# Kernel tuning notes

Hardware: AMD Instinct MI355X
Metric: run time of the kernel (lower is better)

## Reference

```python
import jax, jax.numpy as jnp
import numpy as np

B, E, C, N, NNZ = 64, 100000, 80000, 10000, 1600000
EPS = 1e-5  # GroupLayerNorm eps


def setup_inputs() -> dict:
    key = jax.random.key(0)
    ks = jax.random.split(key, 8)
    x = jax.random.normal(ks[0], (B, E), dtype=jnp.float32)
    # sparse layer nonzero coordinates (graph-structure-constrained weights)
    w_in_rows = jax.random.randint(ks[1], (NNZ,), 0, E)    # edge index (input dim)
    w_in_cols = jax.random.randint(ks[2], (NNZ,), 0, C)    # hidden channel index
    w_out_rows = jax.random.randint(ks[3], (NNZ,), 0, C)   # hidden channel index
    w_out_cols = jax.random.randint(ks[4], (NNZ,), 0, E)   # edge index (output dim)
    # xavier-like scale: avg fan_in per hidden channel ~ NNZ/C
    scale_in = np.sqrt(2.0 / (NNZ / C + NNZ / E)).astype(np.float32)
    v_in = jax.random.normal(ks[5], (NNZ,), dtype=jnp.float32) * scale_in
    v_out = jax.random.normal(ks[6], (NNZ,), dtype=jnp.float32) * scale_in
    b_in = jnp.zeros((C,), jnp.float32)
    b_out = jnp.zeros((E,), jnp.float32)
    gamma = jnp.ones((C,), jnp.float32)   # GroupLayerNorm affine scale (per channel)
    beta = jnp.zeros((C,), jnp.float32)   # GroupLayerNorm affine shift
    channel_groups = jnp.arange(C, dtype=jnp.int64) // (C // N)  # 8 channels per node
    return {
        'x': x, 'v_in': v_in, 'b_in': b_in, 'v_out': v_out, 'b_out': b_out,
        'gamma': gamma, 'beta': beta,
        'w_in_rows': w_in_rows, 'w_in_cols': w_in_cols,
        'w_out_rows': w_out_rows, 'w_out_cols': w_out_cols,
        'channel_groups': channel_groups,
    }


def _sparse_linear(x, rows, cols, values, bias, out_dim):
    # out[b, c] = sum_{k: cols[k]==c} x[b, rows[k]] * values[k] + bias[c]
    contrib = x[:, rows] * values  # [B, nnz]
    out = jnp.zeros((x.shape[0], out_dim), x.dtype).at[:, cols].add(contrib)
    return out + bias


def _group_layer_norm(h, groups, gamma, beta):
    # per-node-group layernorm over that node's channels
    Bsz = h.shape[0]
    counts = jnp.zeros((N,), h.dtype).at[groups].add(1.0)
    gsum = jnp.zeros((Bsz, N), h.dtype).at[:, groups].add(h)
    gsq = jnp.zeros((Bsz, N), h.dtype).at[:, groups].add(h * h)
    mean = gsum / counts
    var = gsq / counts - mean * mean
    hn = (h - mean[:, groups]) * jax.lax.rsqrt(var[:, groups] + EPS)
    return gamma * hn + beta


def reference(x, v_in, b_in, v_out, b_out, gamma, beta,
              w_in_rows, w_in_cols, w_out_rows, w_out_cols, channel_groups):
    # 1. input sparse linear: edges -> hidden channels
    h = _sparse_linear(x, w_in_rows, w_in_cols, v_in, b_in, C)
    # 2. norm_first=True: GroupLayerNorm then nonlinearity (ELU)
    h = _group_layer_norm(h, channel_groups, gamma, beta)
    h = jax.nn.elu(h)
    # 3. output sparse linear: hidden channels -> edges
    out = _sparse_linear(h, w_out_rows, w_out_cols, v_out, b_out, E)
    # 4. dropout p=0 (identity), residual
    return out + x
```

## Files before the change

### kernel.cpp

```cpp
#include <hip/hip_runtime.h>
#include <hip/hip_bf16.h>

#define B_   64
#define E_   100000
#define C_   80000
#define N_   10000
#define GS   8
#define NNZ_ 1600000
#define EPS_ 1e-5f

#define SHIFT 7
#define BK    128
#define NBLK  256
#define CHUNK (NNZ_ / NBLK)
#define NBMAX 800
#define SCAN_CHUNK 1024
#define SORTT 512

__global__ void transpose_x_kernel(const float* __restrict__ x, __hip_bfloat16* __restrict__ xT) {
    __shared__ float tile[64][65];
    const int e0 = blockIdx.x * 64;
    const int t  = threadIdx.x;
    const int c  = t & 63;
    const int r4 = t >> 6;
#pragma unroll
    for (int j = 0; j < 16; ++j) {
        int br = r4 * 16 + j;
        int e  = e0 + c;
        if (e < E_) tile[c][br] = x[br * E_ + e];
    }
    __syncthreads();
#pragma unroll
    for (int j = 0; j < 16; ++j) {
        int er = r4 * 16 + j;
        int e  = e0 + er;
        if (e < E_) xT[e * 64 + c] = __float2bfloat16(tile[er][c]);
    }
}

__global__ __launch_bounds__(SORTT) void count_kernel(const int* __restrict__ cols,
                                                      int* __restrict__ blkcnt, int nb) {
    __shared__ int hist[NBMAX];
    const int t = threadIdx.x;
    for (int j = t; j < nb; j += SORTT) hist[j] = 0;
    __syncthreads();
    const int base = blockIdx.x * CHUNK;
    const int end  = min(NNZ_, base + CHUNK);
    for (int k = base + t; k < end; k += SORTT)
        atomicAdd(&hist[cols[k] >> SHIFT], 1);
    __syncthreads();
    for (int j = t; j < nb; j += SORTT) blkcnt[j * NBLK + blockIdx.x] = hist[j];
}

__global__ void scan_partial_kernel(const int* __restrict__ counts, int* __restrict__ partials,
                                    int dim) {
    __shared__ int red[256];
    const int t    = threadIdx.x;
    const int base = blockIdx.x * SCAN_CHUNK + t * 4;
    int s = 0;
#pragma unroll
    for (int j = 0; j < 4; ++j) { int i = base + j; if (i < dim) s += counts[i]; }
    red[t] = s;
    __syncthreads();
    for (int d = 128; d > 0; d >>= 1) {
        if (t < d) red[t] += red[t + d];
        __syncthreads();
    }
    if (t == 0) partials[blockIdx.x] = red[0];
}

__global__ void scan_base_kernel(int* __restrict__ partials, int nparts) {
    __shared__ int buf[256];
    const int t = threadIdx.x;
    buf[t] = (t < nparts) ? partials[t] : 0;
    __syncthreads();
    for (int d = 1; d < 256; d <<= 1) {
        int v = (t >= d) ? buf[t - d] : 0;
        __syncthreads();
        buf[t] += v;
        __syncthreads();
    }
    if (t < nparts) partials[t] = (t == 0) ? 0 : buf[t - 1];
}

__global__ void scan_emit_kernel(const int* __restrict__ counts, const int* __restrict__ partials,
                                 int* __restrict__ bases, int dim) {
    __shared__ int red[256];
    const int t    = threadIdx.x;
    const int base = blockIdx.x * SCAN_CHUNK + t * 4;
    int v[4];
    int s = 0;
#pragma unroll
    for (int j = 0; j < 4; ++j) {
        int i = base + j;
        v[j] = (i < dim) ? counts[i] : 0;
        s += v[j];
    }
    red[t] = s;
    __syncthreads();
    for (int d = 1; d < 256; d <<= 1) {
        int u = (t >= d) ? red[t - d] : 0;
        __syncthreads();
        red[t] += u;
        __syncthreads();
    }
    int run = partials[blockIdx.x] + ((t == 0) ? 0 : red[t - 1]);
#pragma unroll
    for (int j = 0; j < 4; ++j) {
        int i = base + j;
        if (i < dim) bases[i] = run;
        run += v[j];
    }
}

__global__ __launch_bounds__(SORTT) void place_kernel(const int* __restrict__ rows,
                             const int* __restrict__ cols,
                             const float* __restrict__ vals, const int* __restrict__ bases,
                             uint2* __restrict__ binned, int nb) {
    __shared__ uint2 staged[CHUNK];
    __shared__ unsigned short bof[CHUNK];
    __shared__ int hist[NBMAX];
    __shared__ int cur[NBMAX];
    __shared__ int goff[NBMAX];
    __shared__ int red[SORTT];
    const int t    = threadIdx.x;
    const int blk  = blockIdx.x;
    const int base = blk * CHUNK;
    const int n    = min(NNZ_, base + CHUNK) - base;
    for (int j = t; j < nb; j += SORTT) hist[j] = 0;
    __syncthreads();
    for (int k = t; k < n; k += SORTT) atomicAdd(&hist[cols[base + k] >> SHIFT], 1);
    __syncthreads();
    int lv[2];
    int s = 0;
    const int b0 = t * 2;
#pragma unroll
    for (int j = 0; j < 2; ++j) {
        int idx = b0 + j;
        lv[j] = (idx < nb) ? hist[idx] : 0;
        s += lv[j];
    }
    red[t] = s;
    __syncthreads();
    for (int d = 1; d < SORTT; d <<= 1) {
        int v = (t >= d) ? red[t - d] : 0;
        __syncthreads();
        red[t] += v;
        __syncthreads();
    }
    int run = (t == 0) ? 0 : red[t - 1];
#pragma unroll
    for (int j = 0; j < 2; ++j) {
        int idx = b0 + j;
        if (idx < nb) {
            cur[idx]  = run;
            goff[idx] = bases[idx * NBLK + blk] - run;
        }
        run += lv[j];
    }
    __syncthreads();
    for (int k = t; k < n; k += SORTT) {
        const int c = cols[base + k];
        const int j = c >> SHIFT;
        const int p = atomicAdd(&cur[j], 1);
        staged[p] = make_uint2((unsigned)rows[base + k] | ((unsigned)(c & (BK - 1)) << 17),
                               __float_as_uint(vals[base + k]));
        bof[p] = (unsigned short)j;
    }
    __syncthreads();
    for (int k = t; k < n; k += SORTT) {
        const int j = bof[k];
        binned[goff[j] + k] = staged[k];
    }
}

__global__ __launch_bounds__(SORTT) void binsort_kernel(const uint2* __restrict__ binned,
                               const int* __restrict__ bases,
                               int* __restrict__ offsets, float2* __restrict__ csr,
                               int nb, int dim) {
    __shared__ int hist[BK];
    __shared__ int sc[BK];
    __shared__ int cur[BK];
    const int t   = threadIdx.x;
    const int bkt = blockIdx.x;
    if (t < BK) hist[t] = 0;
    __syncthreads();
    const int beg = bases[bkt * NBLK];
    const int end = (bkt + 1 < nb) ? bases[(bkt + 1) * NBLK] : NNZ_;
    for (int i = beg + t; i < end; i += SORTT)
        atomicAdd(&hist[binned[i].x >> 17], 1);
    __syncthreads();
    if (t < BK) sc[t] = hist[t];
    __syncthreads();
    for (int d = 1; d < BK; d <<= 1) {
        int v = (t < BK && t >= d) ? sc[t - d] : 0;
        __syncthreads();
        if (t < BK) sc[t] += v;
        __syncthreads();
    }
    if (t < BK) {
        const int ex = beg + ((t == 0) ? 0 : sc[t - 1]);
        cur[t] = ex;
        const int c = bkt * BK + t;
        if (c < dim) offsets[c] = ex;
    }
    if (t == 0 && bkt == nb - 1) offsets[dim] = NNZ_;
    __syncthreads();
    for (int i = beg + t; i < end; i += SORTT) {
        const uint2 e = binned[i];
        const int pos = atomicAdd(&cur[e.x >> 17], 1);
        csr[pos] = make_float2(__int_as_float((int)(e.x & 0x1FFFFu)), __uint_as_float(e.y));
    }
}

__device__ __forceinline__ float col_dot(const float2* __restrict__ csr,
                                         const __hip_bfloat16* __restrict__ src,
                                         int beg, int end, int lane, float a0i) {
    float a[16];
    a[0] = a0i;
#pragma unroll
    for (int j = 1; j < 16; ++j) a[j] = 0.f;
    for (int i0 = beg; i0 < end; i0 += 64) {
        const int m = min(64, end - i0);
        float2 mine = make_float2(0.f, 0.f);
        if (lane < m) mine = csr[i0 + lane];
        const int   mr = __float_as_int(mine.x);
        const int   mv = __float_as_int(mine.y);
        int e = 0;
        for (; e + 16 <= m; e += 16) {
#define GSTEP(J)                                                                        \
            {                                                                           \
                const int   r = __builtin_amdgcn_readlane(mr, e + (J));                 \
                const float v = __int_as_float(__builtin_amdgcn_readlane(mv, e + (J))); \
                a[J] = fmaf(v, __bfloat162float(src[r * 64 + lane]), a[J]);             \
            }
            GSTEP(0)  GSTEP(1)  GSTEP(2)  GSTEP(3)
            GSTEP(4)  GSTEP(5)  GSTEP(6)  GSTEP(7)
            GSTEP(8)  GSTEP(9)  GSTEP(10) GSTEP(11)
            GSTEP(12) GSTEP(13) GSTEP(14) GSTEP(15)
        }
        for (; e + 8 <= m; e += 8) {
            GSTEP(0) GSTEP(1) GSTEP(2) GSTEP(3)
            GSTEP(4) GSTEP(5) GSTEP(6) GSTEP(7)
        }
        for (; e < m; ++e) {
            const int   r = __builtin_amdgcn_readlane(mr, e);
            const float v = __int_as_float(__builtin_amdgcn_readlane(mv, e));
            a[0] = fmaf(v, __bfloat162float(src[r * 64 + lane]), a[0]);
        }
#undef GSTEP
    }
    const float s01 = (a[0] + a[1]) + (a[2] + a[3]);
    const float s23 = (a[4] + a[5]) + (a[6] + a[7]);
    const float s45 = (a[8] + a[9]) + (a[10] + a[11]);
    const float s67 = (a[12] + a[13]) + (a[14] + a[15]);
    return (s01 + s23) + (s45 + s67);
}

__global__ __launch_bounds__(256, 8) void gather_kernel(
        const float2* __restrict__ csr, const int* __restrict__ offsets,
        const __hip_bfloat16* __restrict__ src, const float* __restrict__ bias,
        __hip_bfloat16* __restrict__ dst, int dim) {
    const int wave = (blockIdx.x * blockDim.x + threadIdx.x) >> 6;
    const int lane = threadIdx.x & 63;
    if (wave >= dim) return;
    dst[wave * 64 + lane] = __float2bfloat16(
        col_dot(csr, src, offsets[wave], offsets[wave + 1], lane,
                bias ? bias[wave] : 0.f));
}

__global__ void gln_elu_kernel(__hip_bfloat16* __restrict__ h,
                               const float* __restrict__ gamma, const float* __restrict__ beta) {
    const int wave = (blockIdx.x * blockDim.x + threadIdx.x) >> 6;
    const int b    = threadIdx.x & 63;
    if (wave >= N_) return;
    const int c0 = wave * GS;
    float v[GS];
    float s = 0.f, s2 = 0.f;
#pragma unroll
    for (int j = 0; j < GS; ++j) {
        float t = __bfloat162float(h[(c0 + j) * 64 + b]);
        v[j] = t;
        s  += t;
        s2 += t * t;
    }
    const float mean = s * (1.0f / GS);
    const float var  = s2 * (1.0f / GS) - mean * mean;
    const float inv  = rsqrtf(var + EPS_);
#pragma unroll
    for (int j = 0; j < GS; ++j) {
        float hn = (v[j] - mean) * inv;
        float g  = gamma[c0 + j] * hn + beta[c0 + j];
        h[(c0 + j) * 64 + b] = __float2bfloat16((g > 0.f) ? g : expm1f(g));
    }
}

__global__ void finalize_kernel(const __hip_bfloat16* __restrict__ outT,
                                const float* __restrict__ x,
                                const float* __restrict__ b_out, float* __restrict__ out) {
    __shared__ float tile[64][65];
    const int e0 = blockIdx.x * 64;
    const int t  = threadIdx.x;
    const int c  = t & 63;
    const int r4 = t >> 6;
#pragma unroll
    for (int j = 0; j < 16; ++j) {
        int er = r4 * 16 + j;
        int e  = e0 + er;
        if (e < E_) tile[er][c] = __bfloat162float(outT[e * 64 + c]);
    }
    __syncthreads();
#pragma unroll
    for (int j = 0; j < 16; ++j) {
        int br = r4 * 16 + j;
        int e  = e0 + c;
        if (e < E_) out[br * E_ + e] = tile[c][br] + b_out[e] + x[br * E_ + e];
    }
}

extern "C" void kernel_launch(void* const* d_in, const int* in_sizes, int n_in,
                              void* d_out, int out_size, void* d_ws, size_t ws_size,
                              hipStream_t stream) {
    const float* x     = (const float*)d_in[0];
    const float* v_in  = (const float*)d_in[1];
    const float* b_in  = (const float*)d_in[2];
    const float* v_out = (const float*)d_in[3];
    const float* b_out = (const float*)d_in[4];
    const float* gamma = (const float*)d_in[5];
    const float* beta  = (const float*)d_in[6];
    const int* w_in_rows  = (const int*)d_in[7];
    const int* w_in_cols  = (const int*)d_in[8];
    const int* w_out_rows = (const int*)d_in[9];
    const int* w_out_cols = (const int*)d_in[10];
    float* out = (float*)d_out;

    const int nb_C  = (C_ + BK - 1) >> SHIFT;
    const int nb_E  = (E_ + BK - 1) >> SHIFT;
    const int dim_C = nb_C * NBLK;
    const int dim_E = nb_E * NBLK;
    const int np_C  = (dim_C + SCAN_CHUNK - 1) / SCAN_CHUNK;
    const int np_E  = (dim_E + SCAN_CHUNK - 1) / SCAN_CHUNK;

    __hip_bfloat16* xT = (__hip_bfloat16*)d_ws;
    __hip_bfloat16* h  = xT + (size_t)E_ * 64;
    int*    blkcnt   = (int*)(h + (size_t)C_ * 64);
    int*    bases    = blkcnt + dim_E;
    int*    partials = bases + dim_E;
    int*    offsets  = partials + 256;
    uint2*  binned   = (uint2*)(offsets + 100002);
    float2* csr      = (float2*)(binned + NNZ_);

    transpose_x_kernel<<<(E_ + 63) / 64, 256, 0, stream>>>(x, xT);

    count_kernel<<<NBLK, SORTT, 0, stream>>>(w_in_cols, blkcnt, nb_C);
    scan_partial_kernel<<<np_C, 256, 0, stream>>>(blkcnt, partials, dim_C);
    scan_base_kernel<<<1, 256, 0, stream>>>(partials, np_C);
    scan_emit_kernel<<<np_C, 256, 0, stream>>>(blkcnt, partials, bases, dim_C);
    place_kernel<<<NBLK, SORTT, 0, stream>>>(w_in_rows, w_in_cols, v_in, bases, binned, nb_C);
    binsort_kernel<<<nb_C, SORTT, 0, stream>>>(binned, bases, offsets, csr, nb_C, C_);
    gather_kernel<<<(C_ + 3) / 4, 256, 0, stream>>>(csr, offsets, xT, b_in, h, C_);
    gln_elu_kernel<<<(N_ + 3) / 4, 256, 0, stream>>>(h, gamma, beta);

    count_kernel<<<NBLK, SORTT, 0, stream>>>(w_out_cols, blkcnt, nb_E);
    scan_partial_kernel<<<np_E, 256, 0, stream>>>(blkcnt, partials, dim_E);
    scan_base_kernel<<<1, 256, 0, stream>>>(partials, np_E);
    scan_emit_kernel<<<np_E, 256, 0, stream>>>(blkcnt, partials, bases, dim_E);
    place_kernel<<<NBLK, SORTT, 0, stream>>>(w_out_rows, w_out_cols, v_out, bases, binned, nb_E);
    binsort_kernel<<<nb_E, SORTT, 0, stream>>>(binned, bases, offsets, csr, nb_E, E_);
    gather_kernel<<<(E_ + 3) / 4, 256, 0, stream>>>(csr, offsets, h, nullptr, xT, E_);

    finalize_kernel<<<(E_ + 63) / 64, 256, 0, stream>>>(xT, x, b_out, out);
}
```

Measured before the change: 329.9 us.

## Batch both layers' count/scan phases with transpose; stage binsort output in LDS

Merges the x transpose and the column-count histograms for both sparse layers into one prep kernel, and runs the scan kernels for both layers in single launches using separate count/base buffers. This removes several small kernel launches and lets independent work share the GPU. Binsort now scatters into a shared-memory staging buffer when a bucket fits (up to 3072 entries) and then writes coalesced to global memory, with a fallback to the old direct scatter. The prep kernel's larger shared footprint (two 64x65 tiles plus the histogram) may reduce occupancy, and the extra LDS stage adds a barrier.

```diff
diff --git a/kernel.cpp b/kernel.cpp
--- a/kernel.cpp
+++ b/kernel.cpp
@@ -16,47 +16,66 @@
 #define NBMAX 800
 #define SCAN_CHUNK 1024
 #define SORTT 512
-
-__global__ void transpose_x_kernel(const float* __restrict__ x, __hip_bfloat16* __restrict__ xT) {
-    __shared__ float tile[64][65];
-    const int e0 = blockIdx.x * 64;
-    const int t  = threadIdx.x;
-    const int c  = t & 63;
-    const int r4 = t >> 6;
-#pragma unroll
-    for (int j = 0; j < 16; ++j) {
-        int br = r4 * 16 + j;
-        int e  = e0 + c;
-        if (e < E_) tile[c][br] = x[br * E_ + e];
-    }
-    __syncthreads();
-#pragma unroll
-    for (int j = 0; j < 16; ++j) {
-        int er = r4 * 16 + j;
-        int e  = e0 + er;
-        if (e < E_) xT[e * 64 + c] = __float2bfloat16(tile[er][c]);
-    }
-}
-
-__global__ __launch_bounds__(SORTT) void count_kernel(const int* __restrict__ cols,
-                                                      int* __restrict__ blkcnt, int nb) {
+#define NTT   782
+#define BSCAP 3072
+
+__global__ __launch_bounds__(SORTT) void prep_kernel(
+        const float* __restrict__ x, __hip_bfloat16* __restrict__ xT,
+        const int* __restrict__ cols1, int* __restrict__ blkcnt1, int nb1,
+        const int* __restrict__ cols2, int* __restrict__ blkcnt2, int nb2) {
     __shared__ int hist[NBMAX];
+    __shared__ float tile[2][64][65];
+    const int b = blockIdx.x;
     const int t = threadIdx.x;
-    for (int j = t; j < nb; j += SORTT) hist[j] = 0;
-    __syncthreads();
-    const int base = blockIdx.x * CHUNK;
-    const int end  = min(NNZ_, base + CHUNK);
-    for (int k = base + t; k < end; k += SORTT)
-        atomicAdd(&hist[cols[k] >> SHIFT], 1);
-    __syncthreads();
-    for (int j = t; j < nb; j += SORTT) blkcnt[j * NBLK + blockIdx.x] = hist[j];
-}
-
-__global__ void scan_partial_kernel(const int* __restrict__ counts, int* __restrict__ partials,
-                                    int dim) {
+    if (b < 2 * NBLK) {
+        const bool p2 = b >= NBLK;
+        const int* __restrict__ cols = p2 ? cols2 : cols1;
+        int* __restrict__ blkcnt     = p2 ? blkcnt2 : blkcnt1;
+        const int nb  = p2 ? nb2 : nb1;
+        const int blk = p2 ? (b - NBLK) : b;
+        for (int j = t; j < nb; j += SORTT) hist[j] = 0;
+        __syncthreads();
+        const int base = blk * CHUNK;
+        const int end  = min(NNZ_, base + CHUNK);
+        for (int k = base + t; k < end; k += SORTT)
+            atomicAdd(&hist[cols[k] >> SHIFT], 1);
+        __syncthreads();
+        for (int j = t; j < nb; j += SORTT) blkcnt[j * NBLK + blk] = hist[j];
+    } else {
+        const int tb  = b - 2 * NBLK;
+        const int sub = t >> 8;
+        const int tt  = t & 255;
+        const int c   = tt & 63;
+        const int r4  = tt >> 6;
+        const int e0  = tb * 128 + sub * 64;
+#pragma unroll
+        for (int j = 0; j < 16; ++j) {
+            int br = r4 * 16 + j;
+            int e  = e0 + c;
+            if (e < E_) tile[sub][c][br] = x[br * E_ + e];
+        }
+        __syncthreads();
+#pragma unroll
+        for (int j = 0; j < 16; ++j) {
+            int er = r4 * 16 + j;
+            int e  = e0 + er;
+            if (e < E_) xT[e * 64 + c] = __float2bfloat16(tile[sub][er][c]);
+        }
+    }
+}
+
+__global__ void scan_partial_kernel(const int* __restrict__ c1, int* __restrict__ p1,
+                                    int dim1, int np1,
+                                    const int* __restrict__ c2, int* __restrict__ p2,
+                                    int dim2) {
     __shared__ int red[256];
+    const bool ph2 = (int)blockIdx.x >= np1;
+    const int* __restrict__ counts = ph2 ? c2 : c1;
+    int* __restrict__ partials     = ph2 ? p2 : p1;
+    const int dim = ph2 ? dim2 : dim1;
+    const int cb  = ph2 ? (blockIdx.x - np1) : blockIdx.x;
     const int t    = threadIdx.x;
-    const int base = blockIdx.x * SCAN_CHUNK + t * 4;
+    const int base = cb * SCAN_CHUNK + t * 4;
     int s = 0;
 #pragma unroll
     for (int j = 0; j < 4; ++j) { int i = base + j; if (i < dim) s += counts[i]; }
@@ -66,11 +85,14 @@
         if (t < d) red[t] += red[t + d];
         __syncthreads();
     }
-    if (t == 0) partials[blockIdx.x] = red[0];
-}
-
-__global__ void scan_base_kernel(int* __restrict__ partials, int nparts) {
+    if (t == 0) partials[cb] = red[0];
+}
+
+__global__ void scan_base_kernel(int* __restrict__ p1, int np1,
+                                 int* __restrict__ p2, int np2) {
     __shared__ int buf[256];
+    int* __restrict__ partials = blockIdx.x ? p2 : p1;
+    const int nparts           = blockIdx.x ? np2 : np1;
     const int t = threadIdx.x;
     buf[t] = (t < nparts) ? partials[t] : 0;
     __syncthreads();
@@ -83,11 +105,19 @@
     if (t < nparts) partials[t] = (t == 0) ? 0 : buf[t - 1];
 }
 
-__global__ void scan_emit_kernel(const int* __restrict__ counts, const int* __restrict__ partials,
-                                 int* __restrict__ bases, int dim) {
+__global__ void scan_emit_kernel(const int* __restrict__ c1, const int* __restrict__ p1,
+                                 int* __restrict__ b1, int dim1, int np1,
+                                 const int* __restrict__ c2, const int* __restrict__ p2,
+                                 int* __restrict__ b2, int dim2) {
     __shared__ int red[256];
+    const bool ph2 = (int)blockIdx.x >= np1;
+    const int* __restrict__ counts   = ph2 ? c2 : c1;
+    const int* __restrict__ partials = ph2 ? p2 : p1;
+    int* __restrict__ bases          = ph2 ? b2 : b1;
+    const int dim = ph2 ? dim2 : dim1;
+    const int cb  = ph2 ? (blockIdx.x - np1) : blockIdx.x;
     const int t    = threadIdx.x;
-    const int base = blockIdx.x * SCAN_CHUNK + t * 4;
+    const int base = cb * SCAN_CHUNK + t * 4;
     int v[4];
     int s = 0;
 #pragma unroll
@@ -104,7 +134,7 @@
         red[t] += u;
         __syncthreads();
     }
-    int run = partials[blockIdx.x] + ((t == 0) ? 0 : red[t - 1]);
+    int run = partials[cb] + ((t == 0) ? 0 : red[t - 1]);
 #pragma unroll
     for (int j = 0; j < 4; ++j) {
         int i = base + j;
@@ -181,12 +211,14 @@
     __shared__ int hist[BK];
     __shared__ int sc[BK];
     __shared__ int cur[BK];
+    __shared__ float2 stage[BSCAP];
     const int t   = threadIdx.x;
     const int bkt = blockIdx.x;
     if (t < BK) hist[t] = 0;
     __syncthreads();
     const int beg = bases[bkt * NBLK];
     const int end = (bkt + 1 < nb) ? bases[(bkt + 1) * NBLK] : NNZ_;
+    const int cnt = end - beg;
     for (int i = beg + t; i < end; i += SORTT)
         atomicAdd(&hist[binned[i].x >> 17], 1);
     __syncthreads();
@@ -198,18 +230,31 @@
         if (t < BK) sc[t] += v;
         __syncthreads();
     }
+    const bool inlds = (cnt <= BSCAP);
     if (t < BK) {
-        const int ex = beg + ((t == 0) ? 0 : sc[t - 1]);
-        cur[t] = ex;
+        const int exl = (t == 0) ? 0 : sc[t - 1];
+        cur[t] = inlds ? exl : beg + exl;
         const int c = bkt * BK + t;
-        if (c < dim) offsets[c] = ex;
+        if (c < dim) offsets[c] = beg + exl;
     }
     if (t == 0 && bkt == nb - 1) offsets[dim] = NNZ_;
     __syncthreads();
-    for (int i = beg + t; i < end; i += SORTT) {
-        const uint2 e = binned[i];
-        const int pos = atomicAdd(&cur[e.x >> 17], 1);
-        csr[pos] = make_float2(__int_as_float((int)(e.x & 0x1FFFFu)), __uint_as_float(e.y));
+    if (inlds) {
+        for (int i = beg + t; i < end; i += SORTT) {
+            const uint2 e = binned[i];
+            const int pos = atomicAdd(&cur[e.x >> 17], 1);
+            stage[pos] = make_float2(__int_as_float((int)(e.x & 0x1FFFFu)),
+                                     __uint_as_float(e.y));
+        }
+        __syncthreads();
+        for (int k = t; k < cnt; k += SORTT) csr[beg + k] = stage[k];
+    } else {
+        for (int i = beg + t; i < end; i += SORTT) {
+            const uint2 e = binned[i];
+            const int pos = atomicAdd(&cur[e.x >> 17], 1);
+            csr[pos] = make_float2(__int_as_float((int)(e.x & 0x1FFFFu)),
+                                   __uint_as_float(e.y));
+        }
     }
 }
 
@@ -343,30 +388,31 @@
 
     __hip_bfloat16* xT = (__hip_bfloat16*)d_ws;
     __hip_bfloat16* h  = xT + (size_t)E_ * 64;
-    int*    blkcnt   = (int*)(h + (size_t)C_ * 64);
-    int*    bases    = blkcnt + dim_E;
-    int*    partials = bases + dim_E;
-    int*    offsets  = partials + 256;
+    int*    blkcnt1  = (int*)(h + (size_t)C_ * 64);
+    int*    blkcnt2  = blkcnt1 + dim_C;
+    int*    bases1   = blkcnt2 + dim_E;
+    int*    bases2   = bases1 + dim_C;
+    int*    partials1 = bases2 + dim_E;
+    int*    partials2 = partials1 + 256;
+    int*    offsets  = partials2 + 256;
     uint2*  binned   = (uint2*)(offsets + 100002);
     float2* csr      = (float2*)(binned + NNZ_);
 
-    transpose_x_kernel<<<(E_ + 63) / 64, 256, 0, stream>>>(x, xT);
-
-    count_kernel<<<NBLK, SORTT, 0, stream>>>(w_in_cols, blkcnt, nb_C);
-    scan_partial_kernel<<<np_C, 256, 0, stream>>>(blkcnt, partials, dim_C);
-    scan_base_kernel<<<1, 256, 0, stream>>>(partials, np_C);
-    scan_emit_kernel<<<np_C, 256, 0, stream>>>(blkcnt, partials, bases, dim_C);
-    place_kernel<<<NBLK, SORTT, 0, stream>>>(w_in_rows, w_in_cols, v_in, bases, binned, nb_C);
-    binsort_kernel<<<nb_C, SORTT, 0, stream>>>(binned, bases, offsets, csr, nb_C, C_);
+    prep_kernel<<<2 * NBLK + NTT, SORTT, 0, stream>>>(
+        x, xT, w_in_cols, blkcnt1, nb_C, w_out_cols, blkcnt2, nb_E);
+    scan_partial_kernel<<<np_C + np_E, 256, 0, stream>>>(
+        blkcnt1, partials1, dim_C, np_C, blkcnt2, partials2, dim_E);
+    scan_base_kernel<<<2, 256, 0, stream>>>(partials1, np_C, partials2, np_E);
+    scan_emit_kernel<<<np_C + np_E, 256, 0, stream>>>(
+        blkcnt1, partials1, bases1, dim_C, np_C, blkcnt2, partials2, bases2, dim_E);
+
+    place_kernel<<<NBLK, SORTT, 0, stream>>>(w_in_rows, w_in_cols, v_in, bases1, binned, nb_C);
+    binsort_kernel<<<nb_C, SORTT, 0, stream>>>(binned, bases1, offsets, csr, nb_C, C_);
     gather_kernel<<<(C_ + 3) / 4, 256, 0, stream>>>(csr, offsets, xT, b_in, h, C_);
     gln_elu_kernel<<<(N_ + 3) / 4, 256, 0, stream>>>(h, gamma, beta);
 
-    count_kernel<<<NBLK, SORTT, 0, stream>>>(w_out_cols, blkcnt, nb_E);
-    scan_partial_kernel<<<np_E, 256, 0, stream>>>(blkcnt, partials, dim_E);
-    scan_base_kernel<<<1, 256, 0, stream>>>(partials, np_E);
-    scan_emit_kernel<<<np_E, 256, 0, stream>>>(blkcnt, partials, bases, dim_E);
-    place_kernel<<<NBLK, SORTT, 0, stream>>>(w_out_rows, w_out_cols, v_out, bases, binned, nb_E);
-    binsort_kernel<<<nb_E, SORTT, 0, stream>>>(binned, bases, offsets, csr, nb_E, E_);
+    place_kernel<<<NBLK, SORTT, 0, stream>>>(w_out_rows, w_out_cols, v_out, bases2, binned, nb_E);
+    binsort_kernel<<<nb_E, SORTT, 0, stream>>>(binned, bases2, offsets, csr, nb_E, E_);
     gather_kernel<<<(E_ + 3) / 4, 256, 0, stream>>>(csr, offsets, h, nullptr, xT, E_);
 
     finalize_kernel<<<(E_ + 63) / 64, 256, 0, stream>>>(xT, x, b_out, out);
```

New measurement: 310.6 us. 1.06x faster.
